# Kernel optimization log

Hardware: AMD Instinct MI355X
Metric: run time of the kernel (lower is better)

The kernel has to match this reference:

```python
import jax, jax.numpy as jnp
import numpy as np

N_ENT = 14951   # entities (FB15K-style multimodal KG)
N_REL = 1345    # relations == number of context sub-graphs
N_NODES = 120000  # nodes in the batched context graph (b_x length)
N_EDGES = 480000  # edges in the normalized batched adjacency


def _glorot(key, shape):
    scale = np.sqrt(2.0 / (shape[0] + shape[1])).astype(np.float32)
    return jax.random.normal(key, shape, dtype=jnp.float32) * scale


def setup_inputs() -> dict:
    key = jax.random.key(0)
    ks = jax.random.split(key, 16)
    inp = {}
    inp["img_feat"] = jax.random.normal(ks[0], (N_ENT, 4096), dtype=jnp.float32)
    inp["text_feat"] = jax.random.normal(ks[1], (N_ENT, 300), dtype=jnp.float32)
    inp["rel_emb"] = jax.random.normal(ks[2], (N_REL, 300), dtype=jnp.float32)
    # learned parameters (eval mode: dropout = identity)
    inp["W_img_text"] = _glorot(ks[3], (4396, 100)); inp["b_img_text"] = jnp.zeros((100,), jnp.float32)
    inp["W_rel_input"] = _glorot(ks[4], (300, 100)); inp["b_rel_input"] = jnp.zeros((100,), jnp.float32)
    inp["W_gc1"] = _glorot(ks[5], (200, 256)); inp["b_gc1"] = jnp.zeros((256,), jnp.float32)
    inp["W_gc2"] = _glorot(ks[6], (256, 200)); inp["b_gc2"] = jnp.zeros((200,), jnp.float32)
    inp["W_emb"] = _glorot(ks[7], (400, 1)); inp["b_emb"] = jnp.zeros((1,), jnp.float32)
    inp["W_emb_out"] = _glorot(ks[8], (400, 200)); inp["b_emb_out"] = jnp.zeros((200,), jnp.float32)
    inp["W_rel"] = _glorot(ks[9], (300, 200)); inp["b_rel"] = jnp.zeros((200,), jnp.float32)
    # row-normalized adjacency of the batched context graph, as edge list
    inp["edge_weight"] = jax.random.uniform(ks[10], (N_EDGES,), dtype=jnp.float32)
    inp["b_x"] = jax.random.randint(ks[11], (N_NODES,), 0, N_ENT)
    inp["b_graph"] = jax.random.randint(ks[12], (N_NODES,), 0, N_REL)
    inp["edge_src"] = jax.random.randint(ks[13], (N_EDGES,), 0, N_NODES)
    inp["edge_dst"] = jax.random.randint(ks[14], (N_EDGES,), 0, N_NODES)
    return inp


def reference(img_feat, text_feat, rel_emb, W_img_text, b_img_text, W_rel_input,
              b_rel_input, W_gc1, b_gc1, W_gc2, b_gc2, W_emb, b_emb, W_emb_out,
              b_emb_out, W_rel, b_rel, edge_weight, b_x, b_graph, edge_src, edge_dst):
    seg_sum = lambda v, idx, n: jax.ops.segment_sum(v, idx, num_segments=n)

    def spmm(h):  # normalized adjacency @ h via edge-list gather/scatter
        return seg_sum(h[edge_src] * edge_weight[:, None], edge_dst, N_NODES)

    # multimodal entity encoder: Linear(4396 -> 100)
    emf = jnp.concatenate([img_feat, text_feat], axis=1) @ W_img_text + b_img_text
    # relation context encoder: Linear(300 -> 100) + ReLU
    rel_in = jax.nn.relu(rel_emb @ W_rel_input + b_rel_input)
    # batched context-graph node features [M, 200]
    h = jnp.concatenate([emf[b_x], rel_in[b_graph]], axis=1)
    # two-layer GCN encoder (SGCN1)
    h1 = jax.nn.relu(spmm(h @ W_gc1) + b_gc1)
    h2 = spmm(h1 @ W_gc2) + b_gc2          # [M, 200]
    # scatter_mean over entity ids, broadcast back
    cnt = seg_sum(jnp.ones((N_NODES,), h2.dtype), b_x, N_ENT)
    mean = seg_sum(h2, b_x, N_ENT) / jnp.maximum(cnt, 1.0)[:, None]
    emb = jnp.concatenate([h2, mean[b_x]], axis=1)   # [M, 400]
    score = emb @ W_emb + b_emb                      # [M, 1]
    # scatter_softmax over segments b_x (numerically stable)
    smax = jax.ops.segment_max(score, b_x, num_segments=N_ENT)
    e = jnp.exp(score - smax[b_x])
    z_s = e / seg_sum(e, b_x, N_ENT)[b_x]
    new_out = seg_sum(z_s * emb, b_x, N_ENT) @ W_emb_out + b_emb_out  # [N_ENT, 200]
    # relation output encoder: Linear(300 -> 200) + ReLU
    rel_context = jax.nn.relu(rel_emb @ W_rel + b_rel)                # [N_REL, 200]
    return new_out, rel_context
```

## Files before the change

### kernel.cpp

```cpp
#include <hip/hip_runtime.h>

#define N_ENT 14951
#define N_REL 1345
#define NNODE 120000
#define NEDGE 480000
#define MP_ENC 14976
#define KP_ENC 4480
#define NP_ENC 112
#define MROWS1 16320
#define NB_E 118
#define NB_N 15

static inline int ceil_div(int a, int b){ return (a + b - 1) / b; }

typedef __bf16 bf16x8 __attribute__((ext_vector_type(8)));
typedef float f32x4 __attribute__((ext_vector_type(4)));

__device__ inline unsigned short f2bf(float f){
  unsigned u = __float_as_uint(f);
  return (unsigned short)((u + 0x7fffu + ((u >> 16) & 1u)) >> 16);
}
__device__ inline float bf2f(unsigned short b){
  return __uint_as_float(((unsigned)b) << 16);
}

__global__ __launch_bounds__(256) void enc_mfma(
    const float* __restrict__ img, const float* __restrict__ txt,
    const unsigned short* __restrict__ Wt1, float* __restrict__ part)
{
  __shared__ unsigned short As[64 * 40];
  __shared__ unsigned short Bs[112 * 40];
  const int t = threadIdx.x;
  const int m0 = blockIdx.x * 64;
  const int s = blockIdx.y;
  const int l = t & 63, w = t >> 6;
  f32x4 acc[7];
  #pragma unroll
  for (int i = 0; i < 7; i++) acc[i] = f32x4{0.f, 0.f, 0.f, 0.f};

  for (int step = 0; step < 35; ++step) {
    const int kb = s * 1120 + step * 32;
    #pragma unroll
    for (int p = 0; p < 2; ++p) {
      const int c = t + p * 256;
      const int row = c >> 3, kq = c & 7;
      const int rowg = m0 + row;
      const int k = kb + kq * 4;
      float4 v = make_float4(0.f, 0.f, 0.f, 0.f);
      if (rowg < N_ENT) {
        if (k < 4096)      v = *(const float4*)(img + (size_t)rowg * 4096 + k);
        else if (k < 4396) v = *(const float4*)(txt + (size_t)rowg * 300 + (k - 4096));
      }
      ushort4 b;
      b.x = f2bf(v.x); b.y = f2bf(v.y); b.z = f2bf(v.z); b.w = f2bf(v.w);
      *(ushort4*)&As[row * 40 + kq * 4] = b;
    }
    {
      const int n = t >> 2, k16 = t & 3;
      *(uint4*)&Bs[n * 40 + k16 * 8] = *(const uint4*)(Wt1 + (size_t)n * KP_ENC + kb + k16 * 8);
      if (t < 192) {
        const int c = t + 256;
        const int n2 = c >> 2, k2 = c & 3;
        *(uint4*)&Bs[n2 * 40 + k2 * 8] = *(const uint4*)(Wt1 + (size_t)n2 * KP_ENC + kb + k2 * 8);
      }
    }
    __syncthreads();
    bf16x8 a = *(const bf16x8*)&As[(w * 16 + (l & 15)) * 40 + (l >> 4) * 8];
    #pragma unroll
    for (int ct = 0; ct < 7; ++ct) {
      bf16x8 bb = *(const bf16x8*)&Bs[(ct * 16 + (l & 15)) * 40 + (l >> 4) * 8];
      acc[ct] = __builtin_amdgcn_mfma_f32_16x16x32_bf16(a, bb, acc[ct], 0, 0, 0);
    }
    __syncthreads();
  }
  const int rb = m0 + w * 16 + (l >> 4) * 4;
  const int col = l & 15;
  #pragma unroll
  for (int ct = 0; ct < 7; ++ct)
    #pragma unroll
    for (int i = 0; i < 4; ++i)
      part[((size_t)s * MP_ENC + rb + i) * NP_ENC + ct * 16 + col] = acc[ct][i];
}

__global__ __launch_bounds__(256) void enc_reduce(
    const float* __restrict__ part, const float* __restrict__ bias,
    unsigned short* __restrict__ feat1)
{
  int i = blockIdx.x * 256 + threadIdx.x;
  if (i >= N_ENT * 100) return;
  int r = i / 100, c = i % 100;
  float v = bias[c];
  #pragma unroll
  for (int s = 0; s < 4; ++s) v += part[((size_t)s * MP_ENC + r) * NP_ENC + c];
  feat1[(size_t)r * 224 + c] = f2bf(v);
}

__global__ __launch_bounds__(256) void rin_pack(
    const float* __restrict__ rin, unsigned short* __restrict__ feat1)
{
  int i = blockIdx.x * 256 + threadIdx.x;
  if (i >= N_REL * 100) return;
  int r = i / 100, c = i % 100;
  feat1[(size_t)(N_ENT + r) * 224 + 100 + c] = f2bf(rin[i]);
}

__global__ __launch_bounds__(256) void egr1_mfma(
    const unsigned short* __restrict__ feat1, const unsigned short* __restrict__ Wtg1,
    unsigned short* __restrict__ egr1)
{
  __shared__ unsigned short As[64 * 40];
  __shared__ unsigned short Bs[256 * 40];
  const int t = threadIdx.x;
  const int m0 = blockIdx.x * 64;
  const int l = t & 63, w = t >> 6;
  f32x4 acc[16];
  #pragma unroll
  for (int i = 0; i < 16; i++) acc[i] = f32x4{0.f, 0.f, 0.f, 0.f};

  for (int step = 0; step < 7; ++step) {
    const int kb = step * 32;
    {
      const int row = t >> 2, kc = t & 3;
      *(uint4*)&As[row * 40 + kc * 8] = *(const uint4*)(feat1 + (size_t)(m0 + row) * 224 + kb + kc * 8);
    }
    #pragma unroll
    for (int p = 0; p < 4; ++p) {
      const int c = t + p * 256;
      const int n = c >> 2, k16 = c & 3;
      *(uint4*)&Bs[n * 40 + k16 * 8] = *(const uint4*)(Wtg1 + (size_t)n * 224 + kb + k16 * 8);
    }
    __syncthreads();
    bf16x8 a = *(const bf16x8*)&As[(w * 16 + (l & 15)) * 40 + (l >> 4) * 8];
    #pragma unroll
    for (int ct = 0; ct < 16; ++ct) {
      bf16x8 bb = *(const bf16x8*)&Bs[(ct * 16 + (l & 15)) * 40 + (l >> 4) * 8];
      acc[ct] = __builtin_amdgcn_mfma_f32_16x16x32_bf16(a, bb, acc[ct], 0, 0, 0);
    }
    __syncthreads();
  }
  const int rb = m0 + w * 16 + (l >> 4) * 4;
  const int col0 = l & 15;
  #pragma unroll
  for (int ct = 0; ct < 16; ++ct) {
    const int col = ct * 16 + col0;
    #pragma unroll
    for (int i = 0; i < 4; ++i)
      egr1[(size_t)(rb + i) * 256 + col] = f2bf(acc[ct][i]);
  }
}

__global__ __launch_bounds__(256) void gemm2_mfma(
    const unsigned short* __restrict__ h1, const unsigned short* __restrict__ Wt2,
    unsigned short* __restrict__ hg2)
{
  __shared__ unsigned short As[64 * 40];
  __shared__ unsigned short Bs[208 * 40];
  const int t = threadIdx.x;
  const int m0 = blockIdx.x * 64;
  const int l = t & 63, w = t >> 6;
  f32x4 acc[13];
  #pragma unroll
  for (int i = 0; i < 13; i++) acc[i] = f32x4{0.f, 0.f, 0.f, 0.f};

  for (int step = 0; step < 8; ++step) {
    const int kb = step * 32;
    {
      const int row = t >> 2, kc = t & 3;
      *(uint4*)&As[row * 40 + kc * 8] = *(const uint4*)(h1 + (size_t)(m0 + row) * 256 + kb + kc * 8);
    }
    #pragma unroll
    for (int p = 0; p < 4; ++p) {
      const int c = t + p * 256;
      if (c < 832) {
        const int n = c >> 2, k16 = c & 3;
        *(uint4*)&Bs[n * 40 + k16 * 8] = *(const uint4*)(Wt2 + (size_t)n * 256 + kb + k16 * 8);
      }
    }
    __syncthreads();
    bf16x8 a = *(const bf16x8*)&As[(w * 16 + (l & 15)) * 40 + (l >> 4) * 8];
    #pragma unroll
    for (int ct = 0; ct < 13; ++ct) {
      bf16x8 bb = *(const bf16x8*)&Bs[(ct * 16 + (l & 15)) * 40 + (l >> 4) * 8];
      acc[ct] = __builtin_amdgcn_mfma_f32_16x16x32_bf16(a, bb, acc[ct], 0, 0, 0);
    }
    __syncthreads();
  }
  const int rb = m0 + w * 16 + (l >> 4) * 4;
  const int col0 = l & 15;
  #pragma unroll
  for (int ct = 0; ct < 13; ++ct) {
    const int col = ct * 16 + col0;
    #pragma unroll
    for (int i = 0; i < 4; ++i)
      hg2[(size_t)(rb + i) * 208 + col] = f2bf(acc[ct][i]);
  }
}

__global__ __launch_bounds__(256) void fin_mfma(
    const unsigned short* __restrict__ embA, const unsigned short* __restrict__ Wteo,
    const float* __restrict__ b_eo, float* __restrict__ out)
{
  __shared__ unsigned short As[64 * 40];
  __shared__ unsigned short Bs[208 * 40];
  const int t = threadIdx.x;
  const int m0 = blockIdx.x * 64;
  const int l = t & 63, w = t >> 6;
  f32x4 acc[13];
  #pragma unroll
  for (int i = 0; i < 13; i++) acc[i] = f32x4{0.f, 0.f, 0.f, 0.f};

  for (int step = 0; step < 13; ++step) {
    const int kb = step * 32;
    {
      const int row = t >> 2, kc = t & 3;
      *(uint4*)&As[row * 40 + kc * 8] = *(const uint4*)(embA + (size_t)(m0 + row) * 416 + kb + kc * 8);
    }
    #pragma unroll
    for (int p = 0; p < 4; ++p) {
      const int c = t + p * 256;
      if (c < 832) {
        const int n = c >> 2, k16 = c & 3;
        *(uint4*)&Bs[n * 40 + k16 * 8] = *(const uint4*)(Wteo + (size_t)n * 416 + kb + k16 * 8);
      }
    }
    __syncthreads();
    bf16x8 a = *(const bf16x8*)&As[(w * 16 + (l & 15)) * 40 + (l >> 4) * 8];
    #pragma unroll
    for (int ct = 0; ct < 13; ++ct) {
      bf16x8 bb = *(const bf16x8*)&Bs[(ct * 16 + (l & 15)) * 40 + (l >> 4) * 8];
      acc[ct] = __builtin_amdgcn_mfma_f32_16x16x32_bf16(a, bb, acc[ct], 0, 0, 0);
    }
    __syncthreads();
  }
  const int rb = m0 + w * 16 + (l >> 4) * 4;
  const int col0 = l & 15;
  #pragma unroll
  for (int ct = 0; ct < 13; ++ct) {
    const int col = ct * 16 + col0;
    if (col < 200) {
      const float b = b_eo[col];
      #pragma unroll
      for (int i = 0; i < 4; ++i) {
        const int r = rb + i;
        if (r < N_ENT) out[(size_t)r * 200 + col] = acc[ct][i] + b;
      }
    }
  }
}

__global__ __launch_bounds__(256) void wt_all_k(
    const float* __restrict__ W_it, const float* __restrict__ W_g1,
    const float* __restrict__ W_g2, const float* __restrict__ W_eo,
    unsigned short* __restrict__ Wt1, unsigned short* __restrict__ Wtg1,
    unsigned short* __restrict__ Wt2, unsigned short* __restrict__ Wteo)
{
  int i = blockIdx.x * 256 + threadIdx.x;
  if (i < NP_ENC * KP_ENC) {
    int n = i / KP_ENC, k = i % KP_ENC;
    float v = (n < 100 && k < 4396) ? W_it[(size_t)k * 100 + n] : 0.f;
    Wt1[i] = f2bf(v);
    return;
  }
  i -= NP_ENC * KP_ENC;
  if (i < 256 * 224) {
    int n = i / 224, k = i % 224;
    float v = (k < 200) ? W_g1[(size_t)k * 256 + n] : 0.f;
    Wtg1[i] = f2bf(v);
    return;
  }
  i -= 256 * 224;
  if (i < 208 * 256) {
    int n = i >> 8, k = i & 255;
    float v = (n < 200) ? W_g2[(size_t)k * 200 + n] : 0.f;
    Wt2[i] = f2bf(v);
    return;
  }
  i -= 208 * 256;
  if (i < 208 * 416) {
    int n = i / 416, k = i % 416;
    float v = (n < 200 && k < 400) ? W_eo[(size_t)k * 200 + n] : 0.f;
    Wteo[i] = f2bf(v);
  }
}

template<bool RELU, bool HASBIAS>
__global__ __launch_bounds__(256) void gemm_f32(
    const float* __restrict__ A1, int K1, const float* __restrict__ A2,
    const float* __restrict__ B, const float* __restrict__ bias,
    float* __restrict__ C, int M, int K, int N)
{
  constexpr int BM = 64, BN = 128, BK = 16;
  __shared__ float As[BK][BM + 4];
  __shared__ float Bs[BK][BN];
  const int t = threadIdx.x;
  const int m0 = blockIdx.y * BM, n0 = blockIdx.x * BN;
  const int tr = t >> 4, tc = t & 15;
  const int tm0 = tr * 4, tn0 = tc * 8;
  const int K2 = K - K1;
  const int arow = t >> 2, aq = (t & 3) * 4;
  const int brow = t >> 4, bc0 = (t & 15) * 4;
  float acc[4][8];
  #pragma unroll
  for (int i = 0; i < 4; i++)
    #pragma unroll
    for (int j = 0; j < 8; j++) acc[i][j] = 0.f;

  for (int k0 = 0; k0 < K; k0 += BK) {
    {
      const int r = m0 + arow;
      const int k = k0 + aq;
      float4 v = make_float4(0.f, 0.f, 0.f, 0.f);
      if (r < M) {
        if (k + 3 < K1) {
          v = *(const float4*)(A1 + (size_t)r * K1 + k);
        } else if (k >= K1 && (k - K1) + 3 < K2) {
          v = *(const float4*)(A2 + (size_t)r * K2 + (k - K1));
        } else {
          float tmp[4] = {0.f, 0.f, 0.f, 0.f};
          #pragma unroll
          for (int j = 0; j < 4; j++) {
            int kj = k + j;
            if (kj < K) tmp[j] = (kj < K1) ? A1[(size_t)r * K1 + kj]
                                           : A2[(size_t)r * K2 + (kj - K1)];
          }
          v = make_float4(tmp[0], tmp[1], tmp[2], tmp[3]);
        }
      }
      As[aq + 0][arow] = v.x; As[aq + 1][arow] = v.y;
      As[aq + 2][arow] = v.z; As[aq + 3][arow] = v.w;
    }
    {
      const int k = k0 + brow;
      #pragma unroll
      for (int h = 0; h < 2; h++) {
        const int n = n0 + bc0 + h * 64;
        float4 v = make_float4(0.f, 0.f, 0.f, 0.f);
        if (k < K) {
          if (n + 3 < N) {
            v = *(const float4*)(B + (size_t)k * N + n);
          } else {
            float tmp[4] = {0.f, 0.f, 0.f, 0.f};
            for (int j = 0; j < 4; j++) if (n + j < N) tmp[j] = B[(size_t)k * N + n + j];
            v = make_float4(tmp[0], tmp[1], tmp[2], tmp[3]);
          }
        }
        *(float4*)&Bs[brow][bc0 + h * 64] = v;
      }
    }
    __syncthreads();
    #pragma unroll
    for (int k = 0; k < BK; k++) {
      float a[4], b[8];
      *(float4*)&a[0] = *(const float4*)&As[k][tm0];
      *(float4*)&b[0] = *(const float4*)&Bs[k][tn0];
      *(float4*)&b[4] = *(const float4*)&Bs[k][tn0 + 4];
      #pragma unroll
      for (int i = 0; i < 4; i++)
        #pragma unroll
        for (int j = 0; j < 8; j++) acc[i][j] = fmaf(a[i], b[j], acc[i][j]);
    }
    __syncthreads();
  }
  #pragma unroll
  for (int i = 0; i < 4; i++) {
    const int r = m0 + tm0 + i;
    if (r >= M) continue;
    #pragma unroll
    for (int j = 0; j < 8; j++) {
      const int c = n0 + tn0 + j;
      if (c >= N) continue;
      float v = acc[i][j];
      if (HASBIAS) v += bias[c];
      if (RELU) v = fmaxf(v, 0.f);
      C[(size_t)r * N + c] = v;
    }
  }
}

__global__ __launch_bounds__(256) void hist2_k(
    const int* __restrict__ edst, const int* __restrict__ bx,
    int* __restrict__ ehist, int* __restrict__ nhist)
{
  int i = blockIdx.x * 256 + threadIdx.x;
  if (i < NEDGE) { atomicAdd(&ehist[edst[i]], 1); return; }
  i -= NEDGE;
  if (i < NNODE) atomicAdd(&nhist[bx[i]], 1);
}

__global__ __launch_bounds__(256) void scan1_k(
    const int* __restrict__ ehist, int* __restrict__ ebase, int* __restrict__ epart,
    const int* __restrict__ nhist, int* __restrict__ nbase, int* __restrict__ npart)
{
  __shared__ int s[256];
  const int t = threadIdx.x;
  const bool eregion = blockIdx.x < NB_E;
  const int b = eregion ? blockIdx.x : blockIdx.x - NB_E;
  const int n = eregion ? NNODE : N_ENT;
  const int* hist = eregion ? ehist : nhist;
  int* base = eregion ? ebase : nbase;
  int* partial = eregion ? epart : npart;
  const int i0 = b * 1024 + t * 4;
  int v[4];
  #pragma unroll
  for (int j = 0; j < 4; j++) v[j] = (i0 + j < n) ? hist[i0 + j] : 0;
  const int tsum = v[0] + v[1] + v[2] + v[3];
  s[t] = tsum;
  __syncthreads();
  #pragma unroll
  for (int off = 1; off < 256; off <<= 1) {
    int u = (t >= off) ? s[t - off] : 0;
    __syncthreads();
    s[t] += u;
    __syncthreads();
  }
  int run = s[t] - tsum;
  #pragma unroll
  for (int j = 0; j < 4; j++) {
    if (i0 + j < n) base[i0 + j] = run;
    run += v[j];
  }
  if (t == 255) partial[b] = s[255];
}

__global__ __launch_bounds__(256) void scan2_k(
    int* __restrict__ epart, int* __restrict__ ebase_end,
    int* __restrict__ npart, int* __restrict__ nbase_end)
{
  __shared__ int s[256];
  const int t = threadIdx.x;
  const bool eregion = blockIdx.x == 0;
  int* partial = eregion ? epart : npart;
  const int nb = eregion ? NB_E : NB_N;
  const int v = (t < nb) ? partial[t] : 0;
  s[t] = v;
  __syncthreads();
  #pragma unroll
  for (int off = 1; off < 256; off <<= 1) {
    int u = (t >= off) ? s[t - off] : 0;
    __syncthreads();
    s[t] += u;
    __syncthreads();
  }
  if (t < nb) partial[t] = s[t] - v;
  if (t == 255) *(eregion ? ebase_end : nbase_end) = s[255];
}

#define NB3_E 469
__global__ __launch_bounds__(256) void scan3_k(
    int* __restrict__ ebase, const int* __restrict__ epart,
    int* __restrict__ nbase, const int* __restrict__ npart)
{
  if (blockIdx.x < NB3_E) {
    int i = blockIdx.x * 256 + threadIdx.x;
    if (i < NNODE) ebase[i] += epart[i >> 10];
  } else {
    int i = (blockIdx.x - NB3_E) * 256 + threadIdx.x;
    if (i < N_ENT) nbase[i] += npart[i >> 10];
  }
}

__global__ __launch_bounds__(256) void scatter2_k(
    const int* __restrict__ esrc, const int* __restrict__ edst, const float* __restrict__ ew,
    const int* __restrict__ bx, const int* __restrict__ bg,
    const int* __restrict__ ebase, int* __restrict__ ecur,
    float* __restrict__ s_w, int* __restrict__ s_src,
    int* __restrict__ s_en, int* __restrict__ s_gn,
    const int* __restrict__ nbase, int* __restrict__ ncur, int* __restrict__ node_of)
{
  int i = blockIdx.x * 256 + threadIdx.x;
  if (i < NEDGE) {
    int d = edst[i];
    int p = ebase[d] + atomicAdd(&ecur[d], 1);
    int s = esrc[i];
    s_w[p] = ew[i];
    s_src[p] = s;
    s_en[p] = bx[s];
    s_gn[p] = bg[s];
    return;
  }
  i -= NEDGE;
  if (i < NNODE) {
    int ent = bx[i];
    int p = nbase[ent] + atomicAdd(&ncur[ent], 1);
    node_of[p] = i;
  }
}

__global__ __launch_bounds__(256) void spmm1_g(
    const int* __restrict__ ebase, const float* __restrict__ s_w,
    const int* __restrict__ s_en, const int* __restrict__ s_gn,
    const unsigned short* __restrict__ egr1,
    const float* __restrict__ b_g1, unsigned short* __restrict__ h1)
{
  const int gid = blockIdx.x * blockDim.x + threadIdx.x;
  const int d = gid >> 6, lane = gid & 63;
  if (d >= NNODE) return;
  const int p0 = ebase[d], p1 = ebase[d + 1];
  float acc[4] = {0.f, 0.f, 0.f, 0.f};
  for (int p = p0; p < p1; ++p) {
    const float w = s_w[p];
    const int en = s_en[p], gn = s_gn[p];
    const ushort4 va = *(const ushort4*)(egr1 + (size_t)en * 256 + lane * 4);
    const ushort4 vb = *(const ushort4*)(egr1 + (size_t)(N_ENT + gn) * 256 + lane * 4);
    acc[0] += w * (bf2f(va.x) + bf2f(vb.x));
    acc[1] += w * (bf2f(va.y) + bf2f(vb.y));
    acc[2] += w * (bf2f(va.z) + bf2f(vb.z));
    acc[3] += w * (bf2f(va.w) + bf2f(vb.w));
  }
  const float4 b = ((const float4*)b_g1)[lane];
  ushort4 o;
  o.x = f2bf(fmaxf(acc[0] + b.x, 0.f));
  o.y = f2bf(fmaxf(acc[1] + b.y, 0.f));
  o.z = f2bf(fmaxf(acc[2] + b.z, 0.f));
  o.w = f2bf(fmaxf(acc[3] + b.w, 0.f));
  *(ushort4*)(h1 + (size_t)d * 256 + lane * 4) = o;
}

__global__ __launch_bounds__(256) void spmm2_g(
    const int* __restrict__ ebase, const float* __restrict__ s_w,
    const int* __restrict__ s_src, const unsigned short* __restrict__ hg2,
    const float* __restrict__ b_g2, const float* __restrict__ W_e,
    float* __restrict__ h2, float* __restrict__ score)
{
  const int gid = blockIdx.x * blockDim.x + threadIdx.x;
  const int d = gid >> 6, lane = gid & 63;
  if (d >= NNODE) return;
  const int p0 = ebase[d], p1 = ebase[d + 1];
  float acc[4] = {0.f, 0.f, 0.f, 0.f};
  const int col = lane * 4;
  if (lane < 52) {
    for (int p = p0; p < p1; ++p) {
      const float w = s_w[p];
      const ushort4 v = *(const ushort4*)(hg2 + (size_t)s_src[p] * 208 + col);
      acc[0] += w * bf2f(v.x); acc[1] += w * bf2f(v.y);
      acc[2] += w * bf2f(v.z); acc[3] += w * bf2f(v.w);
    }
  }
  float sp = 0.f;
  if (col < 200) {
    const float4 b = ((const float4*)b_g2)[lane];
    acc[0] += b.x; acc[1] += b.y; acc[2] += b.z; acc[3] += b.w;
    *(float4*)(h2 + (size_t)d * 200 + col) = make_float4(acc[0], acc[1], acc[2], acc[3]);
    const float4 we = ((const float4*)W_e)[lane];
    sp = acc[0] * we.x + acc[1] * we.y + acc[2] * we.z + acc[3] * we.w;
  }
  #pragma unroll
  for (int off = 32; off; off >>= 1) sp += __shfl_xor(sp, off);
  if (lane == 0) score[d] = sp;
}

__global__ __launch_bounds__(256) void ent_k(
    const int* __restrict__ nbase, const int* __restrict__ node_of,
    const float* __restrict__ h2, const float* __restrict__ score,
    unsigned short* __restrict__ embA)
{
  const int gid = blockIdx.x * blockDim.x + threadIdx.x;
  const int ent = gid >> 6, lane = gid & 63;
  if (ent >= N_ENT) return;
  const int p0 = nbase[ent], p1 = nbase[ent + 1];
  const int cnt = p1 - p0;
  float m = -3.4e38f;
  for (int p = p0 + lane; p < p1; p += 64) m = fmaxf(m, score[node_of[p]]);
  #pragma unroll
  for (int off = 32; off; off >>= 1) m = fmaxf(m, __shfl_xor(m, off));
  float es = 0.f;
  for (int p = p0 + lane; p < p1; p += 64) es += __expf(score[node_of[p]] - m);
  #pragma unroll
  for (int off = 32; off; off >>= 1) es += __shfl_xor(es, off);
  const float inv_es = (cnt > 0) ? 1.f / es : 0.f;
  const float inv_cnt = 1.f / fmaxf((float)cnt, 1.f);
  float4 aw = make_float4(0.f, 0.f, 0.f, 0.f);
  float4 am = make_float4(0.f, 0.f, 0.f, 0.f);
  for (int p = p0; p < p1; ++p) {
    const int nd = node_of[p];
    const float z = __expf(score[nd] - m) * inv_es;
    if (lane < 50) {
      const float4 v = ((const float4*)(h2 + (size_t)nd * 200))[lane];
      aw.x += z * v.x; aw.y += z * v.y; aw.z += z * v.z; aw.w += z * v.w;
      am.x += v.x; am.y += v.y; am.z += v.z; am.w += v.w;
    }
  }
  if (lane < 50) {
    ushort4 ow, om;
    ow.x = f2bf(aw.x); ow.y = f2bf(aw.y); ow.z = f2bf(aw.z); ow.w = f2bf(aw.w);
    om.x = f2bf(am.x * inv_cnt); om.y = f2bf(am.y * inv_cnt);
    om.z = f2bf(am.z * inv_cnt); om.w = f2bf(am.w * inv_cnt);
    *(ushort4*)(embA + (size_t)ent * 416 + lane * 4) = ow;
    *(ushort4*)(embA + (size_t)ent * 416 + 200 + lane * 4) = om;
  }
}

extern "C" void kernel_launch(void* const* d_in, const int* in_sizes, int n_in,
                              void* d_out, int out_size, void* d_ws, size_t ws_size,
                              hipStream_t stream)
{
  const float* img  = (const float*)d_in[0];
  const float* txt  = (const float*)d_in[1];
  const float* rel  = (const float*)d_in[2];
  const float* W_it = (const float*)d_in[3];
  const float* b_it = (const float*)d_in[4];
  const float* W_ri = (const float*)d_in[5];
  const float* b_ri = (const float*)d_in[6];
  const float* W_g1 = (const float*)d_in[7];
  const float* b_g1 = (const float*)d_in[8];
  const float* W_g2 = (const float*)d_in[9];
  const float* b_g2 = (const float*)d_in[10];
  const float* W_e  = (const float*)d_in[11];
  const float* W_eo = (const float*)d_in[13];
  const float* b_eo = (const float*)d_in[14];
  const float* W_r  = (const float*)d_in[15];
  const float* b_r  = (const float*)d_in[16];
  const float* ew   = (const float*)d_in[17];
  const int*   bx   = (const int*)d_in[18];
  const int*   bg   = (const int*)d_in[19];
  const int*   esrc = (const int*)d_in[20];
  const int*   edst = (const int*)d_in[21];

  float* ws = (float*)d_ws;
  size_t off = 0;
  auto alloc = [&](size_t n){ size_t r = off; off += (n + 255) & ~(size_t)255; return r; };
  unsigned short* feat1 = (unsigned short*)(ws + alloc((size_t)MROWS1 * 224 / 2));
  unsigned short* egr1  = (unsigned short*)(ws + alloc((size_t)MROWS1 * 256 / 2));
  unsigned short* h1    = (unsigned short*)(ws + alloc((size_t)NNODE * 256 / 2));
  unsigned short* hg2   = (unsigned short*)(ws + alloc((size_t)NNODE * 208 / 2));
  unsigned short* embA  = (unsigned short*)(ws + alloc((size_t)MP_ENC * 416 / 2));
  float* h2    = ws + alloc((size_t)NNODE * 200);
  float* rin   = ws + alloc((size_t)N_REL * 100);
  float* score = ws + alloc(NNODE);
  size_t cnt0 = alloc((size_t)NNODE * 2 + (size_t)N_ENT * 2);
  int* ehist = (int*)(ws + cnt0);
  int* ecur  = ehist + NNODE;
  int* nhist = ecur + NNODE;
  int* ncur  = nhist + N_ENT;
  int* ebase = (int*)(ws + alloc(NNODE + 1));
  int* nbase = (int*)(ws + alloc(N_ENT + 1));
  int* epart = (int*)(ws + alloc(256));
  int* npart = (int*)(ws + alloc(256));
  float* s_w  = ws + alloc(NEDGE);
  int* s_src  = (int*)(ws + alloc(NEDGE));
  int* s_en   = (int*)(ws + alloc(NEDGE));
  int* s_gn   = (int*)(ws + alloc(NEDGE));
  int* node_of = (int*)(ws + alloc(NNODE));
  unsigned short* Wt1  = (unsigned short*)(ws + alloc((size_t)NP_ENC * KP_ENC / 2));
  unsigned short* Wtg1 = (unsigned short*)(ws + alloc((size_t)256 * 224 / 2));
  unsigned short* Wt2  = (unsigned short*)(ws + alloc((size_t)208 * 256 / 2));
  unsigned short* Wteo = (unsigned short*)(ws + alloc((size_t)208 * 416 / 2));
  float* part = h2;

  dim3 blk(256);

  hipMemsetAsync(ehist, 0, ((size_t)NNODE * 2 + (size_t)N_ENT * 2) * 4, stream);
  hipMemsetAsync(feat1, 0, (size_t)MROWS1 * 224 * 2, stream);
  hipMemsetAsync(embA,  0, (size_t)MP_ENC * 416 * 2, stream);

  hist2_k<<<ceil_div(NEDGE + NNODE, 256), blk, 0, stream>>>(edst, bx, ehist, nhist);
  scan1_k<<<NB_E + NB_N, blk, 0, stream>>>(ehist, ebase, epart, nhist, nbase, npart);
  scan2_k<<<2, blk, 0, stream>>>(epart, ebase + NNODE, npart, nbase + N_ENT);
  scan3_k<<<NB3_E + ceil_div(N_ENT, 256), blk, 0, stream>>>(ebase, epart, nbase, npart);
  scatter2_k<<<ceil_div(NEDGE + NNODE, 256), blk, 0, stream>>>(
      esrc, edst, ew, bx, bg, ebase, ecur, s_w, s_src, s_en, s_gn, nbase, ncur, node_of);

  wt_all_k<<<ceil_div(NP_ENC * KP_ENC + 256 * 224 + 208 * 256 + 208 * 416, 256), blk, 0, stream>>>(
      W_it, W_g1, W_g2, W_eo, Wt1, Wtg1, Wt2, Wteo);

  enc_mfma<<<dim3(MP_ENC / 64, 4), blk, 0, stream>>>(img, txt, Wt1, part);
  enc_reduce<<<ceil_div(N_ENT * 100, 256), blk, 0, stream>>>(part, b_it, feat1);
  gemm_f32<true, true><<<dim3(1, ceil_div(N_REL, 64)), blk, 0, stream>>>(
      rel, 300, rel, W_ri, b_ri, rin, N_REL, 300, 100);
  rin_pack<<<ceil_div(N_REL * 100, 256), blk, 0, stream>>>(rin, feat1);

  egr1_mfma<<<MROWS1 / 64, blk, 0, stream>>>(feat1, Wtg1, egr1);
  spmm1_g<<<ceil_div(NNODE * 64, 256), blk, 0, stream>>>(
      ebase, s_w, s_en, s_gn, egr1, b_g1, h1);

  gemm2_mfma<<<NNODE / 64, blk, 0, stream>>>(h1, Wt2, hg2);
  spmm2_g<<<ceil_div(NNODE * 64, 256), blk, 0, stream>>>(
      ebase, s_w, s_src, hg2, b_g2, W_e, h2, score);

  ent_k<<<ceil_div(N_ENT * 64, 256), blk, 0, stream>>>(nbase, node_of, h2, score, embA);

  float* out_new = (float*)d_out;
  float* out_rel = out_new + (size_t)N_ENT * 200;
  fin_mfma<<<MP_ENC / 64, blk, 0, stream>>>(embA, Wteo, b_eo, out_new);
  gemm_f32<true, true><<<dim3(2, ceil_div(N_REL, 64)), blk, 0, stream>>>(
      rel, 300, rel, W_r, b_r, out_rel, N_REL, 300, 200);
}
```

Measured before the change: 618.1 us.

## Restructure encoder GEMM with resident B slice, direct A loads, higher split-K

The encoder GEMM kernel now loads its whole weight K-slice into shared memory once per block. Each lane reads its A fragment straight from global memory into registers, converting to bf16 there, with a two-stage software prefetch. This removes the per-step shared-memory round trip and the barriers around it. Split-K goes from 4 to 8, which gives more blocks and more partials for enc_reduce to sum, and the partials get their own buffer. Separately, h2 is now stored as bf16, halving the traffic between spmm2 and ent_k at some cost in precision.

```diff
diff --git a/kernel.cpp b/kernel.cpp
--- a/kernel.cpp
+++ b/kernel.cpp
@@ -5,8 +5,12 @@
 #define NNODE 120000
 #define NEDGE 480000
 #define MP_ENC 14976
-#define KP_ENC 4480
+#define KP_ENC 4608
 #define NP_ENC 112
+#define ENC_SPLIT 8
+#define ENC_KSPLIT 576
+#define ENC_STEPS 18
+#define ENC_LDSTRIDE 584
 #define MROWS1 16320
 #define NB_E 118
 #define NB_N 15
@@ -15,6 +19,7 @@
 
 typedef __bf16 bf16x8 __attribute__((ext_vector_type(8)));
 typedef float f32x4 __attribute__((ext_vector_type(4)));
+union U8 { unsigned short u[8]; bf16x8 v; };
 
 __device__ inline unsigned short f2bf(float f){
   unsigned u = __float_as_uint(f);
@@ -28,58 +33,78 @@
     const float* __restrict__ img, const float* __restrict__ txt,
     const unsigned short* __restrict__ Wt1, float* __restrict__ part)
 {
-  __shared__ unsigned short As[64 * 40];
-  __shared__ unsigned short Bs[112 * 40];
+  __shared__ unsigned short Bs[112 * ENC_LDSTRIDE];
   const int t = threadIdx.x;
-  const int m0 = blockIdx.x * 64;
+  const int w = t >> 6, l = t & 63;
   const int s = blockIdx.y;
-  const int l = t & 63, w = t >> 6;
+  const int row16 = blockIdx.x * 64 + w * 16;
+  int row = row16 + (l & 15);
+  if (row >= N_ENT) row = N_ENT - 1;
+  const int koff = (l >> 4) * 8;
+
+  for (int idx = t; idx < 112 * 72; idx += 256) {
+    const int col = idx / 72, kc = idx - col * 72;
+    *(uint4*)&Bs[col * ENC_LDSTRIDE + kc * 8] =
+        *(const uint4*)(Wt1 + (size_t)col * KP_ENC + s * ENC_KSPLIT + kc * 8);
+  }
+  __syncthreads();
+
   f32x4 acc[7];
   #pragma unroll
   for (int i = 0; i < 7; i++) acc[i] = f32x4{0.f, 0.f, 0.f, 0.f};
 
-  for (int step = 0; step < 35; ++step) {
-    const int kb = s * 1120 + step * 32;
-    #pragma unroll
-    for (int p = 0; p < 2; ++p) {
-      const int c = t + p * 256;
-      const int row = c >> 3, kq = c & 7;
-      const int rowg = m0 + row;
-      const int k = kb + kq * 4;
-      float4 v = make_float4(0.f, 0.f, 0.f, 0.f);
-      if (rowg < N_ENT) {
-        if (k < 4096)      v = *(const float4*)(img + (size_t)rowg * 4096 + k);
-        else if (k < 4396) v = *(const float4*)(txt + (size_t)rowg * 300 + (k - 4096));
+  const float* irow = img + (size_t)row * 4096;
+  const float* trow = txt + (size_t)row * 300;
+  const int kbase = s * ENC_KSPLIT + koff;
+
+  auto loadA = [&](int step, float4& u0, float4& u1) {
+    u0 = make_float4(0.f, 0.f, 0.f, 0.f);
+    u1 = make_float4(0.f, 0.f, 0.f, 0.f);
+    if (step < ENC_STEPS) {
+      const int c = kbase + step * 32;
+      if (c + 8 <= 4096) {
+        u0 = *(const float4*)(irow + c);
+        u1 = *(const float4*)(irow + c + 4);
+      } else if (c >= 4096) {
+        const int ct_ = c - 4096;
+        if (ct_ <= 288) {
+          u0 = *(const float4*)(trow + ct_);
+          u1 = *(const float4*)(trow + ct_ + 4);
+        } else if (ct_ == 296) {
+          u0 = *(const float4*)(trow + 296);
+        }
       }
-      ushort4 b;
-      b.x = f2bf(v.x); b.y = f2bf(v.y); b.z = f2bf(v.z); b.w = f2bf(v.w);
-      *(ushort4*)&As[row * 40 + kq * 4] = b;
-    }
-    {
-      const int n = t >> 2, k16 = t & 3;
-      *(uint4*)&Bs[n * 40 + k16 * 8] = *(const uint4*)(Wt1 + (size_t)n * KP_ENC + kb + k16 * 8);
-      if (t < 192) {
-        const int c = t + 256;
-        const int n2 = c >> 2, k2 = c & 3;
-        *(uint4*)&Bs[n2 * 40 + k2 * 8] = *(const uint4*)(Wt1 + (size_t)n2 * KP_ENC + kb + k2 * 8);
-      }
-    }
-    __syncthreads();
-    bf16x8 a = *(const bf16x8*)&As[(w * 16 + (l & 15)) * 40 + (l >> 4) * 8];
+    }
+  };
+  auto compute = [&](int step, const float4& u0, const float4& u1) {
+    U8 pa;
+    pa.u[0] = f2bf(u0.x); pa.u[1] = f2bf(u0.y); pa.u[2] = f2bf(u0.z); pa.u[3] = f2bf(u0.w);
+    pa.u[4] = f2bf(u1.x); pa.u[5] = f2bf(u1.y); pa.u[6] = f2bf(u1.z); pa.u[7] = f2bf(u1.w);
+    const bf16x8 a = pa.v;
+    const int kl = step * 32 + koff;
     #pragma unroll
     for (int ct = 0; ct < 7; ++ct) {
-      bf16x8 bb = *(const bf16x8*)&Bs[(ct * 16 + (l & 15)) * 40 + (l >> 4) * 8];
-      acc[ct] = __builtin_amdgcn_mfma_f32_16x16x32_bf16(a, bb, acc[ct], 0, 0, 0);
-    }
-    __syncthreads();
-  }
-  const int rb = m0 + w * 16 + (l >> 4) * 4;
-  const int col = l & 15;
+      const bf16x8 b = *(const bf16x8*)&Bs[(ct * 16 + (l & 15)) * ENC_LDSTRIDE + kl];
+      acc[ct] = __builtin_amdgcn_mfma_f32_16x16x32_bf16(a, b, acc[ct], 0, 0, 0);
+    }
+  };
+
+  float4 a0, a1, b0, b1;
+  loadA(0, a0, a1);
+  for (int step = 0; step < ENC_STEPS; step += 2) {
+    loadA(step + 1, b0, b1);
+    compute(step, a0, a1);
+    loadA(step + 2, a0, a1);
+    compute(step + 1, b0, b1);
+  }
+
+  const int orow = row16 + (koff >> 1);
+  float* pp = part + (size_t)s * MP_ENC * NP_ENC;
   #pragma unroll
   for (int ct = 0; ct < 7; ++ct)
     #pragma unroll
     for (int i = 0; i < 4; ++i)
-      part[((size_t)s * MP_ENC + rb + i) * NP_ENC + ct * 16 + col] = acc[ct][i];
+      pp[(size_t)(orow + i) * NP_ENC + ct * 16 + (l & 15)] = acc[ct][i];
 }
 
 __global__ __launch_bounds__(256) void enc_reduce(
@@ -91,7 +116,7 @@
   int r = i / 100, c = i % 100;
   float v = bias[c];
   #pragma unroll
-  for (int s = 0; s < 4; ++s) v += part[((size_t)s * MP_ENC + r) * NP_ENC + c];
+  for (int s = 0; s < ENC_SPLIT; ++s) v += part[((size_t)s * MP_ENC + r) * NP_ENC + c];
   feat1[(size_t)r * 224 + c] = f2bf(v);
 }
 
@@ -520,7 +545,7 @@
     const int* __restrict__ ebase, const float* __restrict__ s_w,
     const int* __restrict__ s_src, const unsigned short* __restrict__ hg2,
     const float* __restrict__ b_g2, const float* __restrict__ W_e,
-    float* __restrict__ h2, float* __restrict__ score)
+    unsigned short* __restrict__ h2, float* __restrict__ score)
 {
   const int gid = blockIdx.x * blockDim.x + threadIdx.x;
   const int d = gid >> 6, lane = gid & 63;
@@ -528,19 +553,19 @@
   const int p0 = ebase[d], p1 = ebase[d + 1];
   float acc[4] = {0.f, 0.f, 0.f, 0.f};
   const int col = lane * 4;
-  if (lane < 52) {
+  float sp = 0.f;
+  if (lane < 50) {
     for (int p = p0; p < p1; ++p) {
       const float w = s_w[p];
       const ushort4 v = *(const ushort4*)(hg2 + (size_t)s_src[p] * 208 + col);
       acc[0] += w * bf2f(v.x); acc[1] += w * bf2f(v.y);
       acc[2] += w * bf2f(v.z); acc[3] += w * bf2f(v.w);
     }
-  }
-  float sp = 0.f;
-  if (col < 200) {
     const float4 b = ((const float4*)b_g2)[lane];
     acc[0] += b.x; acc[1] += b.y; acc[2] += b.z; acc[3] += b.w;
-    *(float4*)(h2 + (size_t)d * 200 + col) = make_float4(acc[0], acc[1], acc[2], acc[3]);
+    ushort4 o;
+    o.x = f2bf(acc[0]); o.y = f2bf(acc[1]); o.z = f2bf(acc[2]); o.w = f2bf(acc[3]);
+    *(ushort4*)(h2 + (size_t)d * 200 + col) = o;
     const float4 we = ((const float4*)W_e)[lane];
     sp = acc[0] * we.x + acc[1] * we.y + acc[2] * we.z + acc[3] * we.w;
   }
@@ -551,7 +576,7 @@
 
 __global__ __launch_bounds__(256) void ent_k(
     const int* __restrict__ nbase, const int* __restrict__ node_of,
-    const float* __restrict__ h2, const float* __restrict__ score,
+    const unsigned short* __restrict__ h2, const float* __restrict__ score,
     unsigned short* __restrict__ embA)
 {
   const int gid = blockIdx.x * blockDim.x + threadIdx.x;
@@ -569,22 +594,23 @@
   for (int off = 32; off; off >>= 1) es += __shfl_xor(es, off);
   const float inv_es = (cnt > 0) ? 1.f / es : 0.f;
   const float inv_cnt = 1.f / fmaxf((float)cnt, 1.f);
-  float4 aw = make_float4(0.f, 0.f, 0.f, 0.f);
-  float4 am = make_float4(0.f, 0.f, 0.f, 0.f);
+  float aw[4] = {0.f, 0.f, 0.f, 0.f};
+  float am[4] = {0.f, 0.f, 0.f, 0.f};
   for (int p = p0; p < p1; ++p) {
     const int nd = node_of[p];
     const float z = __expf(score[nd] - m) * inv_es;
     if (lane < 50) {
-      const float4 v = ((const float4*)(h2 + (size_t)nd * 200))[lane];
-      aw.x += z * v.x; aw.y += z * v.y; aw.z += z * v.z; aw.w += z * v.w;
-      am.x += v.x; am.y += v.y; am.z += v.z; am.w += v.w;
+      const ushort4 v = *(const ushort4*)(h2 + (size_t)nd * 200 + lane * 4);
+      const float vx = bf2f(v.x), vy = bf2f(v.y), vz = bf2f(v.z), vw = bf2f(v.w);
+      aw[0] += z * vx; aw[1] += z * vy; aw[2] += z * vz; aw[3] += z * vw;
+      am[0] += vx; am[1] += vy; am[2] += vz; am[3] += vw;
     }
   }
   if (lane < 50) {
     ushort4 ow, om;
-    ow.x = f2bf(aw.x); ow.y = f2bf(aw.y); ow.z = f2bf(aw.z); ow.w = f2bf(aw.w);
-    om.x = f2bf(am.x * inv_cnt); om.y = f2bf(am.y * inv_cnt);
-    om.z = f2bf(am.z * inv_cnt); om.w = f2bf(am.w * inv_cnt);
+    ow.x = f2bf(aw[0]); ow.y = f2bf(aw[1]); ow.z = f2bf(aw[2]); ow.w = f2bf(aw[3]);
+    om.x = f2bf(am[0] * inv_cnt); om.y = f2bf(am[1] * inv_cnt);
+    om.z = f2bf(am[2] * inv_cnt); om.w = f2bf(am[3] * inv_cnt);
     *(ushort4*)(embA + (size_t)ent * 416 + lane * 4) = ow;
     *(ushort4*)(embA + (size_t)ent * 416 + 200 + lane * 4) = om;
   }
@@ -624,7 +650,8 @@
   unsigned short* h1    = (unsigned short*)(ws + alloc((size_t)NNODE * 256 / 2));
   unsigned short* hg2   = (unsigned short*)(ws + alloc((size_t)NNODE * 208 / 2));
   unsigned short* embA  = (unsigned short*)(ws + alloc((size_t)MP_ENC * 416 / 2));
-  float* h2    = ws + alloc((size_t)NNODE * 200);
+  unsigned short* h2    = (unsigned short*)(ws + alloc((size_t)NNODE * 200 / 2));
+  float* part  = ws + alloc((size_t)ENC_SPLIT * MP_ENC * NP_ENC);
   float* rin   = ws + alloc((size_t)N_REL * 100);
   float* score = ws + alloc(NNODE);
   size_t cnt0 = alloc((size_t)NNODE * 2 + (size_t)N_ENT * 2);
@@ -645,7 +672,6 @@
   unsigned short* Wtg1 = (unsigned short*)(ws + alloc((size_t)256 * 224 / 2));
   unsigned short* Wt2  = (unsigned short*)(ws + alloc((size_t)208 * 256 / 2));
   unsigned short* Wteo = (unsigned short*)(ws + alloc((size_t)208 * 416 / 2));
-  float* part = h2;
 
   dim3 blk(256);
 
@@ -663,7 +689,7 @@
   wt_all_k<<<ceil_div(NP_ENC * KP_ENC + 256 * 224 + 208 * 256 + 208 * 416, 256), blk, 0, stream>>>(
       W_it, W_g1, W_g2, W_eo, Wt1, Wtg1, Wt2, Wteo);
 
-  enc_mfma<<<dim3(MP_ENC / 64, 4), blk, 0, stream>>>(img, txt, Wt1, part);
+  enc_mfma<<<dim3(MP_ENC / 64, ENC_SPLIT), blk, 0, stream>>>(img, txt, Wt1, part);
   enc_reduce<<<ceil_div(N_ENT * 100, 256), blk, 0, stream>>>(part, b_it, feat1);
   gemm_f32<true, true><<<dim3(1, ceil_div(N_REL, 64)), blk, 0, stream>>>(
       rel, 300, rel, W_ri, b_ri, rin, N_REL, 300, 100);
```

Result: slower. 677.9 us (+9.7%).

## Raise encoder split-K to 16 and store h2 in bf16

Applied to the files above, without the earlier changes.

The encoder GEMM's split-K factor goes from 4 to 16, with K padded to 4608 and 9 steps per split. This launches far more blocks so more CUs stay busy on the 14951x4396 input. The partial-sum buffer now gets its own, much larger allocation, which adds write and reduce traffic in enc_reduce. Separately, h2 is stored as bf16 instead of fp32, halving the gather traffic in ent_k at some cost in precision.

```diff
diff --git a/kernel.cpp b/kernel.cpp
--- a/kernel.cpp
+++ b/kernel.cpp
@@ -5,8 +5,11 @@
 #define NNODE 120000
 #define NEDGE 480000
 #define MP_ENC 14976
-#define KP_ENC 4480
+#define KP_ENC 4608
 #define NP_ENC 112
+#define ENC_SPLIT 16
+#define ENC_KSPLIT 288
+#define ENC_STEPS 9
 #define MROWS1 16320
 #define NB_E 118
 #define NB_N 15
@@ -38,8 +41,8 @@
   #pragma unroll
   for (int i = 0; i < 7; i++) acc[i] = f32x4{0.f, 0.f, 0.f, 0.f};
 
-  for (int step = 0; step < 35; ++step) {
-    const int kb = s * 1120 + step * 32;
+  for (int step = 0; step < ENC_STEPS; ++step) {
+    const int kb = s * ENC_KSPLIT + step * 32;
     #pragma unroll
     for (int p = 0; p < 2; ++p) {
       const int c = t + p * 256;
@@ -75,11 +78,12 @@
   }
   const int rb = m0 + w * 16 + (l >> 4) * 4;
   const int col = l & 15;
+  float* pp = part + (size_t)s * MP_ENC * NP_ENC;
   #pragma unroll
   for (int ct = 0; ct < 7; ++ct)
     #pragma unroll
     for (int i = 0; i < 4; ++i)
-      part[((size_t)s * MP_ENC + rb + i) * NP_ENC + ct * 16 + col] = acc[ct][i];
+      pp[(size_t)(rb + i) * NP_ENC + ct * 16 + col] = acc[ct][i];
 }
 
 __global__ __launch_bounds__(256) void enc_reduce(
@@ -91,7 +95,7 @@
   int r = i / 100, c = i % 100;
   float v = bias[c];
   #pragma unroll
-  for (int s = 0; s < 4; ++s) v += part[((size_t)s * MP_ENC + r) * NP_ENC + c];
+  for (int s = 0; s < ENC_SPLIT; ++s) v += part[((size_t)s * MP_ENC + r) * NP_ENC + c];
   feat1[(size_t)r * 224 + c] = f2bf(v);
 }
 
@@ -520,7 +524,7 @@
     const int* __restrict__ ebase, const float* __restrict__ s_w,
     const int* __restrict__ s_src, const unsigned short* __restrict__ hg2,
     const float* __restrict__ b_g2, const float* __restrict__ W_e,
-    float* __restrict__ h2, float* __restrict__ score)
+    unsigned short* __restrict__ h2, float* __restrict__ score)
 {
   const int gid = blockIdx.x * blockDim.x + threadIdx.x;
   const int d = gid >> 6, lane = gid & 63;
@@ -528,19 +532,19 @@
   const int p0 = ebase[d], p1 = ebase[d + 1];
   float acc[4] = {0.f, 0.f, 0.f, 0.f};
   const int col = lane * 4;
-  if (lane < 52) {
+  float sp = 0.f;
+  if (lane < 50) {
     for (int p = p0; p < p1; ++p) {
       const float w = s_w[p];
       const ushort4 v = *(const ushort4*)(hg2 + (size_t)s_src[p] * 208 + col);
       acc[0] += w * bf2f(v.x); acc[1] += w * bf2f(v.y);
       acc[2] += w * bf2f(v.z); acc[3] += w * bf2f(v.w);
     }
-  }
-  float sp = 0.f;
-  if (col < 200) {
     const float4 b = ((const float4*)b_g2)[lane];
     acc[0] += b.x; acc[1] += b.y; acc[2] += b.z; acc[3] += b.w;
-    *(float4*)(h2 + (size_t)d * 200 + col) = make_float4(acc[0], acc[1], acc[2], acc[3]);
+    ushort4 o;
+    o.x = f2bf(acc[0]); o.y = f2bf(acc[1]); o.z = f2bf(acc[2]); o.w = f2bf(acc[3]);
+    *(ushort4*)(h2 + (size_t)d * 200 + col) = o;
     const float4 we = ((const float4*)W_e)[lane];
     sp = acc[0] * we.x + acc[1] * we.y + acc[2] * we.z + acc[3] * we.w;
   }
@@ -551,7 +555,7 @@
 
 __global__ __launch_bounds__(256) void ent_k(
     const int* __restrict__ nbase, const int* __restrict__ node_of,
-    const float* __restrict__ h2, const float* __restrict__ score,
+    const unsigned short* __restrict__ h2, const float* __restrict__ score,
     unsigned short* __restrict__ embA)
 {
   const int gid = blockIdx.x * blockDim.x + threadIdx.x;
@@ -569,22 +573,23 @@
   for (int off = 32; off; off >>= 1) es += __shfl_xor(es, off);
   const float inv_es = (cnt > 0) ? 1.f / es : 0.f;
   const float inv_cnt = 1.f / fmaxf((float)cnt, 1.f);
-  float4 aw = make_float4(0.f, 0.f, 0.f, 0.f);
-  float4 am = make_float4(0.f, 0.f, 0.f, 0.f);
+  float aw[4] = {0.f, 0.f, 0.f, 0.f};
+  float am[4] = {0.f, 0.f, 0.f, 0.f};
   for (int p = p0; p < p1; ++p) {
     const int nd = node_of[p];
     const float z = __expf(score[nd] - m) * inv_es;
     if (lane < 50) {
-      const float4 v = ((const float4*)(h2 + (size_t)nd * 200))[lane];
-      aw.x += z * v.x; aw.y += z * v.y; aw.z += z * v.z; aw.w += z * v.w;
-      am.x += v.x; am.y += v.y; am.z += v.z; am.w += v.w;
+      const ushort4 v = *(const ushort4*)(h2 + (size_t)nd * 200 + lane * 4);
+      const float vx = bf2f(v.x), vy = bf2f(v.y), vz = bf2f(v.z), vw = bf2f(v.w);
+      aw[0] += z * vx; aw[1] += z * vy; aw[2] += z * vz; aw[3] += z * vw;
+      am[0] += vx; am[1] += vy; am[2] += vz; am[3] += vw;
     }
   }
   if (lane < 50) {
     ushort4 ow, om;
-    ow.x = f2bf(aw.x); ow.y = f2bf(aw.y); ow.z = f2bf(aw.z); ow.w = f2bf(aw.w);
-    om.x = f2bf(am.x * inv_cnt); om.y = f2bf(am.y * inv_cnt);
-    om.z = f2bf(am.z * inv_cnt); om.w = f2bf(am.w * inv_cnt);
+    ow.x = f2bf(aw[0]); ow.y = f2bf(aw[1]); ow.z = f2bf(aw[2]); ow.w = f2bf(aw[3]);
+    om.x = f2bf(am[0] * inv_cnt); om.y = f2bf(am[1] * inv_cnt);
+    om.z = f2bf(am[2] * inv_cnt); om.w = f2bf(am[3] * inv_cnt);
     *(ushort4*)(embA + (size_t)ent * 416 + lane * 4) = ow;
     *(ushort4*)(embA + (size_t)ent * 416 + 200 + lane * 4) = om;
   }
@@ -624,7 +629,8 @@
   unsigned short* h1    = (unsigned short*)(ws + alloc((size_t)NNODE * 256 / 2));
   unsigned short* hg2   = (unsigned short*)(ws + alloc((size_t)NNODE * 208 / 2));
   unsigned short* embA  = (unsigned short*)(ws + alloc((size_t)MP_ENC * 416 / 2));
-  float* h2    = ws + alloc((size_t)NNODE * 200);
+  unsigned short* h2    = (unsigned short*)(ws + alloc((size_t)NNODE * 200 / 2));
+  float* part  = ws + alloc((size_t)ENC_SPLIT * MP_ENC * NP_ENC);
   float* rin   = ws + alloc((size_t)N_REL * 100);
   float* score = ws + alloc(NNODE);
   size_t cnt0 = alloc((size_t)NNODE * 2 + (size_t)N_ENT * 2);
@@ -645,7 +651,6 @@
   unsigned short* Wtg1 = (unsigned short*)(ws + alloc((size_t)256 * 224 / 2));
   unsigned short* Wt2  = (unsigned short*)(ws + alloc((size_t)208 * 256 / 2));
   unsigned short* Wteo = (unsigned short*)(ws + alloc((size_t)208 * 416 / 2));
-  float* part = h2;
 
   dim3 blk(256);
 
@@ -663,7 +668,7 @@
   wt_all_k<<<ceil_div(NP_ENC * KP_ENC + 256 * 224 + 208 * 256 + 208 * 416, 256), blk, 0, stream>>>(
       W_it, W_g1, W_g2, W_eo, Wt1, Wtg1, Wt2, Wteo);
 
-  enc_mfma<<<dim3(MP_ENC / 64, 4), blk, 0, stream>>>(img, txt, Wt1, part);
+  enc_mfma<<<dim3(MP_ENC / 64, ENC_SPLIT), blk, 0, stream>>>(img, txt, Wt1, part);
   enc_reduce<<<ceil_div(N_ENT * 100, 256), blk, 0, stream>>>(part, b_it, feat1);
   gemm_f32<true, true><<<dim3(1, ceil_div(N_REL, 64)), blk, 0, stream>>>(
       rel, 300, rel, W_ri, b_ri, rin, N_REL, 300, 100);
```

Measured after the change: 629.0 us. Within noise of the previous version (+1.8%).
